# Kernel tuning notes

Measured on AMD Instinct MI355X. Metric: run time of the kernel, lower is better.

Reference implementation:

```python
import jax, jax.numpy as jnp
import numpy as np

# dims: B batch, N tokens (64x64 grid), D slot/feature dim, H heads, HD head_dim
B, N, D = 32, 4096, 256
H, HD = 4, 64            # H * HD == qkv_size == D
S = 16                   # num slots
GH = 128                 # grid-encoder MLP hidden size
MH = 1024                # slot MLP hidden size
NUM_ITER = 3
EPS = 1e-8               # module epsilon
LN_EPS = 1e-6            # flax LayerNorm default


def _ln(x, s, b):
    m = jnp.mean(x, -1, keepdims=True)
    v = jnp.mean(jnp.square(x - m), -1, keepdims=True)
    return (x - m) * jax.lax.rsqrt(v + LN_EPS) * s + b


def setup_inputs() -> dict:
    key = jax.random.key(0)
    ks = jax.random.split(key, 16)
    g = lambda i, shape, scale: jax.random.normal(ks[i], shape, jnp.float32) * scale
    return {
        "slots": g(0, (B, S, D), 1.0),
        "inputs": g(1, (B, N, D + 2), 1.0),  # last 2 channels = coordinate grid
        "ln_in_s": jnp.ones((D,), jnp.float32), "ln_in_b": jnp.zeros((D,), jnp.float32),
        "Wk": g(2, (D, H, HD), D ** -0.5),
        "Wv": g(3, (D, H, HD), D ** -0.5),
        "Wp": g(4, (2, H, HD), 0.5),
        "ge_ln_s": jnp.ones((HD,), jnp.float32), "ge_ln_b": jnp.zeros((HD,), jnp.float32),
        "ge_W1": g(5, (HD, GH), HD ** -0.5), "ge_b1": jnp.zeros((GH,), jnp.float32),
        "ge_W2": g(6, (GH, HD), GH ** -0.5), "ge_b2": jnp.zeros((HD,), jnp.float32),
        "lnq_s": jnp.ones((D,), jnp.float32), "lnq_b": jnp.zeros((D,), jnp.float32),
        "Wq": g(7, (D, H, HD), D ** -0.5),
        "Wo": g(8, (H, HD, D), D ** -0.5),
        "gru_Wi": g(9, (D, 3 * D), D ** -0.5), "gru_bi": jnp.zeros((3 * D,), jnp.float32),
        "gru_Wh": g(10, (D, 3 * D), D ** -0.5), "gru_bhn": jnp.zeros((D,), jnp.float32),
        "mlp_ln_s": jnp.ones((D,), jnp.float32), "mlp_ln_b": jnp.zeros((D,), jnp.float32),
        "mlp_W1": g(11, (D, MH), D ** -0.5), "mlp_b1": jnp.zeros((MH,), jnp.float32),
        "mlp_W2": g(12, (MH, D), MH ** -0.5), "mlp_b2": jnp.zeros((D,), jnp.float32),
    }


def reference(slots, inputs, ln_in_s, ln_in_b, Wk, Wv, Wp, ge_ln_s, ge_ln_b,
              ge_W1, ge_b1, ge_W2, ge_b2, lnq_s, lnq_b, Wq, Wo,
              gru_Wi, gru_bi, gru_Wh, gru_bhn,
              mlp_ln_s, mlp_ln_b, mlp_W1, mlp_b1, mlp_W2, mlp_b2):
    feats, grid = inputs[..., :-2], inputs[..., -2:]
    x = _ln(feats, ln_in_s, ln_in_b)                         # [B,N,D] input pre-norm

    def grid_enc(y):                                          # MLP, pre-LN, no residual
        h = _ln(y, ge_ln_s, ge_ln_b)
        h = jax.nn.relu(h @ ge_W1 + ge_b1)
        return h @ ge_W2 + ge_b2

    p = jnp.einsum('bng,ghe->bnhe', grid, Wp)                 # grid projector
    k = grid_enc(jnp.einsum('bnd,dhe->bnhe', x, Wk) + p)      # [B,N,H,HD]
    v = grid_enc(jnp.einsum('bnd,dhe->bnhe', x, Wv) + p)      # [B,N,H,HD]

    scale = HD ** -0.5
    for _ in range(NUM_ITER):
        sn = _ln(slots, lnq_s, lnq_b)
        q = jnp.einsum('bsd,dhe->bshe', sn, Wq) * scale       # [B,S,H,HD]
        attn = jnp.einsum('bqhe,bkhe->bhqk', q, k)            # [B,H,S,N]
        attn = jax.nn.softmax(attn, axis=-2)                  # inverted: over slots
        attn = attn / (jnp.sum(attn, -1, keepdims=True) + EPS)  # renormalize over keys
        upd = jnp.einsum('bhqk,bkhe->bqhe', attn, v)          # [B,S,H,HD]
        upd = jnp.einsum('bqhe,hed->bqd', upd, Wo)            # multi-head merge -> [B,S,D]
        # flax GRUCell: hidden = slots, input = upd
        gi = upd @ gru_Wi + gru_bi
        gh = slots @ gru_Wh
        ir, iz, inn = jnp.split(gi, 3, -1)
        hr, hz, hn = jnp.split(gh, 3, -1)
        r = jax.nn.sigmoid(ir + hr)
        z = jax.nn.sigmoid(iz + hz)
        n = jnp.tanh(inn + r * (hn + gru_bhn))
        slots = (1.0 - z) * n + z * slots
        # residual pre-LN MLP
        h = _ln(slots, mlp_ln_s, mlp_ln_b)
        h = jax.nn.relu(h @ mlp_W1 + mlp_b1) @ mlp_W2 + mlp_b2
        slots = slots + h
    return slots
```

## Files before the change

### kernel.cpp

```cpp
#include <hip/hip_runtime.h>

using u16 = unsigned short;
using u32 = unsigned int;

#define Bn 32
#define Nn 4096
#define Dn 256
#define Hn 4
#define HDn 64
#define Sn 16

typedef __bf16 bf16x8 __attribute__((ext_vector_type(8)));
typedef float  f32x4  __attribute__((ext_vector_type(4)));

#define MFMA16(a,b,c) __builtin_amdgcn_mfma_f32_16x16x32_bf16((a),(b),(c),0,0,0)

__device__ __forceinline__ float bf2f(u16 u){ u32 x=((u32)u)<<16; float f; __builtin_memcpy(&f,&x,4); return f; }
__device__ __forceinline__ u16 f2bf(float f){ __bf16 h=(__bf16)f; u16 u; __builtin_memcpy(&u,&h,2); return u; }
__device__ __forceinline__ u32 pack2(float a,float b){ return (u32)f2bf(a)|((u32)f2bf(b)<<16); }
__device__ __forceinline__ float sigm(float x){ x=fminf(fmaxf(x,-30.f),30.f); return 1.f/(1.f+__expf(-x)); }
__device__ __forceinline__ float tanhfast(float x){ x=fminf(fmaxf(x,-15.f),15.f); float t=__expf(-2.f*x); return (1.f-t)/(1.f+t); }
__device__ __forceinline__ float gld(const void* p, int idx, bool f32){
  return f32 ? ((const float*)p)[idx] : bf2f(((const u16*)p)[idx]);
}
__device__ __forceinline__ bool is_f32(const u32* flagw){ return *flagw == 0x3F800000u; }

#define PB_LNS 0
#define PB_LNB 256
#define PB_WP 512
#define PB_GES 1024
#define PB_GEB 1088
#define PB_GB1 1152
#define PB_GB2 1280
#define PB_LQS 1344
#define PB_LQB 1600
#define PB_GBI 1856
#define PB_GBHN 2624
#define PB_MLS 2880
#define PB_MLB 3136
#define PB_MB1 3392
#define PB_MB2 4416
#define PB_TOT 4672

__global__ __launch_bounds__(256) void k_prep(
  const void* __restrict__ Wk, const void* __restrict__ Wv,
  const void* __restrict__ gW1, const void* __restrict__ gW2,
  const void* __restrict__ Wq, const void* __restrict__ Wo,
  const void* __restrict__ Wi, const void* __restrict__ Wh,
  const void* __restrict__ mW1, const void* __restrict__ mW2,
  const void* __restrict__ slots_in,
  const void* __restrict__ ln_s, const void* __restrict__ ln_b, const void* __restrict__ Wp,
  const void* __restrict__ ge_s, const void* __restrict__ ge_b,
  const void* __restrict__ geb1, const void* __restrict__ geb2,
  const void* __restrict__ lnqs, const void* __restrict__ lnqb,
  const void* __restrict__ gbi, const void* __restrict__ gbhn,
  const void* __restrict__ mls, const void* __restrict__ mlb,
  const void* __restrict__ mb1, const void* __restrict__ mb2,
  u16* __restrict__ Wcat_t, u16* __restrict__ Wq_t, u16* __restrict__ W1t,
  u16* __restrict__ W2t, u16* __restrict__ Wo_t, u16* __restrict__ Wi_t,
  u16* __restrict__ Wh_t, u16* __restrict__ mW1t, u16* __restrict__ mW2t,
  float* __restrict__ slots_cur, float* __restrict__ pb)
{
  bool f32 = is_f32((const u32*)ln_s);
  int idx = blockIdx.x*256 + threadIdx.x;
  if (idx < 65536){ int o=idx>>8,d=idx&255; Wcat_t[idx]=f2bf(gld(Wk,d*256+o,f32)); return; } idx-=65536;
  if (idx < 65536){ int o=idx>>8,d=idx&255; Wcat_t[65536+idx]=f2bf(gld(Wv,d*256+o,f32)); return; } idx-=65536;
  if (idx < 8192){ int n=idx>>6,k=idx&63; W1t[idx]=f2bf(gld(gW1,k*128+n,f32)); return; } idx-=8192;
  if (idx < 8192){ int n=idx>>7,k=idx&127; W2t[idx]=f2bf(gld(gW2,k*64+n,f32)); return; } idx-=8192;
  if (idx < 65536){ int o=idx>>8,d=idx&255; Wq_t[idx]=f2bf(gld(Wq,d*256+o,f32)); return; } idx-=65536;
  if (idx < 65536){ int d=idx>>8,he=idx&255; Wo_t[idx]=f2bf(gld(Wo,he*256+d,f32)); return; } idx-=65536;
  if (idx < 196608){ int n=idx>>8,k=idx&255; Wi_t[idx]=f2bf(gld(Wi,k*768+n,f32)); return; } idx-=196608;
  if (idx < 196608){ int n=idx>>8,k=idx&255; Wh_t[idx]=f2bf(gld(Wh,k*768+n,f32)); return; } idx-=196608;
  if (idx < 262144){ int n=idx>>8,k=idx&255; mW1t[idx]=f2bf(gld(mW1,k*1024+n,f32)); return; } idx-=262144;
  if (idx < 262144){ int n=idx>>10,k=idx&1023; mW2t[idx]=f2bf(gld(mW2,k*256+n,f32)); return; } idx-=262144;
  if (idx < 131072){ slots_cur[idx]=gld(slots_in,idx,f32); return; } idx-=131072;
  if (idx < 256){ pb[PB_LNS+idx]=gld(ln_s,idx,f32); return; } idx-=256;
  if (idx < 256){ pb[PB_LNB+idx]=gld(ln_b,idx,f32); return; } idx-=256;
  if (idx < 512){ pb[PB_WP+idx]=gld(Wp,idx,f32); return; } idx-=512;
  if (idx < 64){ pb[PB_GES+idx]=gld(ge_s,idx,f32); return; } idx-=64;
  if (idx < 64){ pb[PB_GEB+idx]=gld(ge_b,idx,f32); return; } idx-=64;
  if (idx < 128){ pb[PB_GB1+idx]=gld(geb1,idx,f32); return; } idx-=128;
  if (idx < 64){ pb[PB_GB2+idx]=gld(geb2,idx,f32); return; } idx-=64;
  if (idx < 256){ pb[PB_LQS+idx]=gld(lnqs,idx,f32); return; } idx-=256;
  if (idx < 256){ pb[PB_LQB+idx]=gld(lnqb,idx,f32); return; } idx-=256;
  if (idx < 768){ pb[PB_GBI+idx]=gld(gbi,idx,f32); return; } idx-=768;
  if (idx < 256){ pb[PB_GBHN+idx]=gld(gbhn,idx,f32); return; } idx-=256;
  if (idx < 256){ pb[PB_MLS+idx]=gld(mls,idx,f32); return; } idx-=256;
  if (idx < 256){ pb[PB_MLB+idx]=gld(mlb,idx,f32); return; } idx-=256;
  if (idx < 1024){ pb[PB_MB1+idx]=gld(mb1,idx,f32); return; } idx-=1024;
  if (idx < 256){ pb[PB_MB2+idx]=gld(mb2,idx,f32); return; }
}

__global__ __launch_bounds__(256) void k_feat(
  const void* __restrict__ inputs, const u32* __restrict__ flagw,
  const float* __restrict__ pb,
  const u16* __restrict__ Wcat_t, const u16* __restrict__ W1t_g, const u16* __restrict__ W2t_g,
  u16* __restrict__ Kb, u16* __restrict__ Vb)
{
  __shared__ __align__(16) char sm[56832];
  u16* x_lds = (u16*)sm;
  u16* kp    = (u16*)(sm+16896);
  u16* h_b   = (u16*)(sm+33792);
  u16* stg   = (u16*)(sm+33792);
  float* misc= (float*)(sm+51200);
  float* lnS = misc;      float* lnB = misc+256;
  float* wp0 = misc+512;  float* wp1 = misc+768;
  float* geS = misc+1024; float* geB = misc+1088;
  float* gB1 = misc+1152; float* gB2 = misc+1280;
  float* gxy = misc+1344;

  int tid = threadIdx.x;
  int batch = blockIdx.x >> 7;
  int n0 = (blockIdx.x & 127) << 5;
  bool f32 = is_f32(flagw);

  lnS[tid]=pb[PB_LNS+tid]; lnB[tid]=pb[PB_LNB+tid];
  wp0[tid]=pb[PB_WP+tid];  wp1[tid]=pb[PB_WP+256+tid];
  if (tid < 64){ geS[tid]=pb[PB_GES+tid]; geB[tid]=pb[PB_GEB+tid]; gB2[tid]=pb[PB_GB2+tid]; }
  if (tid < 128) gB1[tid]=pb[PB_GB1+tid];
  __syncthreads();

  {
    int row = tid>>3, seg = tid&7;
    size_t rowbase = ((size_t)(batch*Nn + n0 + row))*258;
    float v[32]; float sum=0.f, ssq=0.f;
    if (f32){
      const float2* ip = (const float2*)((const float*)inputs + rowbase + seg*32);
      #pragma unroll
      for (int i=0;i<16;i++){ float2 t=ip[i]; v[2*i]=t.x; v[2*i+1]=t.y; sum+=t.x+t.y; ssq+=t.x*t.x+t.y*t.y; }
      if (seg==0){
        const float* gp = (const float*)inputs + rowbase + 256;
        gxy[row*2]=gp[0]; gxy[row*2+1]=gp[1];
      }
    } else {
      const u32* ip = (const u32*)inputs + ((rowbase + seg*32)>>1);
      #pragma unroll
      for (int i=0;i<16;i++){ u32 u=ip[i]; float a=bf2f((u16)(u&0xffff)), b=bf2f((u16)(u>>16));
        v[2*i]=a; v[2*i+1]=b; sum+=a+b; ssq+=a*a+b*b; }
      if (seg==0){
        u32 u = *((const u32*)inputs + ((rowbase + 256)>>1));
        gxy[row*2]=bf2f((u16)(u&0xffff)); gxy[row*2+1]=bf2f((u16)(u>>16));
      }
    }
    sum += __shfl_xor(sum,1); sum += __shfl_xor(sum,2); sum += __shfl_xor(sum,4);
    ssq += __shfl_xor(ssq,1); ssq += __shfl_xor(ssq,2); ssq += __shfl_xor(ssq,4);
    float m = sum*(1.f/256.f);
    float var = ssq*(1.f/256.f) - m*m;
    float rs = rsqrtf(var + 1e-6f);
    u32* xw = (u32*)(x_lds + row*264 + seg*32);
    #pragma unroll
    for (int i=0;i<16;i++){
      int c = seg*32 + 2*i;
      float a=(v[2*i]-m)*rs*lnS[c]+lnB[c];
      float b=(v[2*i+1]-m)*rs*lnS[c+1]+lnB[c+1];
      xw[i]=pack2(a,b);
    }
  }
  __syncthreads();

  int wv = tid>>6, lane = tid&63, quad = lane>>4, l15 = lane&15;

  for (int pass=0; pass<2; pass++){
    f32x4 acc[2][4];
    #pragma unroll
    for (int mi=0;mi<2;mi++)
      #pragma unroll
      for (int j=0;j<4;j++) acc[mi][j]=(f32x4){0,0,0,0};
    const u16* Bbase = Wcat_t + pass*65536;
    #pragma unroll
    for (int ks=0; ks<8; ks++){
      bf16x8 a[2], bb[4];
      #pragma unroll
      for (int mi=0;mi<2;mi++) a[mi] = *(const bf16x8*)(x_lds + (mi*16+l15)*264 + ks*32 + quad*8);
      #pragma unroll
      for (int j=0;j<4;j++) bb[j] = *(const bf16x8*)(Bbase + ((wv*4+j)*16+l15)*256 + ks*32 + quad*8);
      #pragma unroll
      for (int mi=0;mi<2;mi++)
        #pragma unroll
        for (int j=0;j<4;j++) acc[mi][j] = MFMA16(a[mi], bb[j], acc[mi][j]);
    }
    #pragma unroll
    for (int j=0;j<4;j++){
      int col = wv*64 + j*16 + l15;
      float w0 = wp0[col], w1 = wp1[col];
      #pragma unroll
      for (int mi=0;mi<2;mi++)
        #pragma unroll
        for (int r=0;r<4;r++){
          int rw = mi*16 + quad*4 + r;
          float val = acc[mi][j][r] + gxy[rw*2]*w0 + gxy[rw*2+1]*w1;
          kp[rw*264 + col] = f2bf(val);
        }
    }
    __syncthreads();

    {
      int g = tid>>1, halfe = tid&1;
      int token = g>>2, hd = g&3;
      u32* ptr = (u32*)(kp + token*264 + hd*64 + halfe*32);
      float vv[32]; float sum=0.f, ssq=0.f;
      #pragma unroll
      for (int i=0;i<16;i++){ u32 u=ptr[i]; float a=bf2f((u16)(u&0xffff)), b=bf2f((u16)(u>>16));
        vv[2*i]=a; vv[2*i+1]=b; sum+=a+b; ssq+=a*a+b*b; }
      sum += __shfl_xor(sum,1); ssq += __shfl_xor(ssq,1);
      float m = sum*(1.f/64.f);
      float var = ssq*(1.f/64.f) - m*m;
      float rs = rsqrtf(var + 1e-6f);
      #pragma unroll
      for (int i=0;i<16;i++){
        int e = halfe*32 + 2*i;
        float a=(vv[2*i]-m)*rs*geS[e]+geB[e];
        float b=(vv[2*i+1]-m)*rs*geS[e+1]+geB[e+1];
        ptr[i]=pack2(a,b);
      }
    }
    __syncthreads();

    int mtb = (wv>>1)*2;
    for (int half=0; half<2; half++){
      int hbase = half*64;
      int ntb = (wv&1)*4;
      f32x4 e1[2][4];
      #pragma unroll
      for (int mi=0;mi<2;mi++)
        #pragma unroll
        for (int nj=0;nj<4;nj++) e1[mi][nj]=(f32x4){0,0,0,0};
      #pragma unroll
      for (int ks=0; ks<2; ks++){
        bf16x8 a[2], bb[4];
        #pragma unroll
        for (int mi=0;mi<2;mi++){
          int g = hbase + (mtb+mi)*16 + l15;
          a[mi] = *(const bf16x8*)(kp + (g>>2)*264 + (g&3)*64 + ks*32 + quad*8);
        }
        #pragma unroll
        for (int nj=0;nj<4;nj++) bb[nj] = *(const bf16x8*)(W1t_g + ((ntb+nj)*16+l15)*64 + ks*32 + quad*8);
        #pragma unroll
        for (int mi=0;mi<2;mi++)
          #pragma unroll
          for (int nj=0;nj<4;nj++) e1[mi][nj] = MFMA16(a[mi], bb[nj], e1[mi][nj]);
      }
      #pragma unroll
      for (int nj=0;nj<4;nj++){
        int col = (ntb+nj)*16 + l15;
        float b1 = gB1[col];
        #pragma unroll
        for (int mi=0;mi<2;mi++)
          #pragma unroll
          for (int r=0;r<4;r++){
            int rw = (mtb+mi)*16 + quad*4 + r;
            h_b[rw*136 + col] = f2bf(fmaxf(e1[mi][nj][r]+b1, 0.f));
          }
      }
      __syncthreads();
      int ntb2 = (wv&1)*2;
      f32x4 e2[2][2];
      #pragma unroll
      for (int mi=0;mi<2;mi++)
        #pragma unroll
        for (int nj=0;nj<2;nj++) e2[mi][nj]=(f32x4){0,0,0,0};
      #pragma unroll
      for (int ks=0; ks<4; ks++){
        bf16x8 a[2], bb[2];
        #pragma unroll
        for (int mi=0;mi<2;mi++) a[mi] = *(const bf16x8*)(h_b + ((mtb+mi)*16+l15)*136 + ks*32 + quad*8);
        #pragma unroll
        for (int nj=0;nj<2;nj++) bb[nj] = *(const bf16x8*)(W2t_g + ((ntb2+nj)*16+l15)*128 + ks*32 + quad*8);
        #pragma unroll
        for (int mi=0;mi<2;mi++)
          #pragma unroll
          for (int nj=0;nj<2;nj++) e2[mi][nj] = MFMA16(a[mi], bb[nj], e2[mi][nj]);
      }
      __syncthreads();
      #pragma unroll
      for (int nj=0;nj<2;nj++){
        int e = (ntb2+nj)*16 + l15;
        float b2 = gB2[e];
        #pragma unroll
        for (int mi=0;mi<2;mi++)
          #pragma unroll
          for (int r=0;r<4;r++){
            int g = hbase + (mtb+mi)*16 + quad*4 + r;
            int hd = g&3, rowl = (g>>2)&15;
            float val = e2[mi][nj][r] + b2;
            if (pass==0) stg[hd*16*72 + rowl*72 + e] = f2bf(val);
            else         stg[hd*64*24 + e*24 + rowl] = f2bf(val);
          }
      }
      __syncthreads();
      if (pass==0){
        int hd = tid>>6, rowl = (tid>>2)&15, sg = tid&3;
        const uint4* s = (const uint4*)(stg + hd*1152 + rowl*72 + sg*16);
        uint4 q0 = s[0], q1 = s[1];
        u16* dst = Kb + ((size_t)((batch*Hn+hd)*Nn + n0 + half*16 + rowl))*64 + sg*16;
        ((uint4*)dst)[0]=q0; ((uint4*)dst)[1]=q1;
      } else {
        int hd = tid>>6, e = tid&63;
        const uint4* s = (const uint4*)(stg + hd*1536 + e*24);
        uint4 q0 = s[0], q1 = s[1];
        u16* dst = Vb + ((size_t)((batch*Hn+hd)*HDn + e))*Nn + n0 + half*16;
        ((uint4*)dst)[0]=q0; ((uint4*)dst)[1]=q1;
      }
      __syncthreads();
    }
  }
}

__global__ __launch_bounds__(256) void k_attn(
  const float* __restrict__ slots_cur, const float* __restrict__ pb,
  const u16* __restrict__ Wq_t, const u16* __restrict__ Kb, const u16* __restrict__ Vb,
  float* __restrict__ num_part, float* __restrict__ den_part)
{
  __shared__ u16 sn[16*264];
  __shared__ u16 qld[16*72];
  __shared__ u16 pld[4][16*40];
  int tid = threadIdx.x;
  int chunk = blockIdx.x, h = blockIdx.y, b = blockIdx.z;

  {
    int rowq = tid>>4, li = tid&15;
    const float* sp = slots_cur + ((size_t)(b*16+rowq))*256 + li*16;
    float v[16]; float sum=0.f, ssq=0.f;
    #pragma unroll
    for (int i=0;i<16;i++){ float x=sp[i]; v[i]=x; sum+=x; ssq+=x*x; }
    sum += __shfl_xor(sum,1); sum += __shfl_xor(sum,2); sum += __shfl_xor(sum,4); sum += __shfl_xor(sum,8);
    ssq += __shfl_xor(ssq,1); ssq += __shfl_xor(ssq,2); ssq += __shfl_xor(ssq,4); ssq += __shfl_xor(ssq,8);
    float m = sum*(1.f/256.f);
    float var = ssq*(1.f/256.f) - m*m;
    float rs = rsqrtf(var + 1e-6f);
    u32* dst = (u32*)(sn + rowq*264 + li*16);
    #pragma unroll
    for (int i=0;i<8;i++){
      int c = li*16 + 2*i;
      float a=(v[2*i]-m)*rs*pb[PB_LQS+c]+pb[PB_LQB+c];
      float bval=(v[2*i+1]-m)*rs*pb[PB_LQS+c+1]+pb[PB_LQB+c+1];
      dst[i]=pack2(a,bval);
    }
  }
  __syncthreads();

  int wv = tid>>6, lane = tid&63, quad = lane>>4, l15 = lane&15;
  {
    f32x4 qa = (f32x4){0,0,0,0};
    #pragma unroll
    for (int ks=0; ks<8; ks++){
      bf16x8 a = *(const bf16x8*)(sn + l15*264 + ks*32 + quad*8);
      bf16x8 bb = *(const bf16x8*)(Wq_t + (h*64 + wv*16 + l15)*256 + ks*32 + quad*8);
      qa = MFMA16(a, bb, qa);
    }
    #pragma unroll
    for (int r=0;r<4;r++) qld[(quad*4+r)*72 + wv*16 + l15] = f2bf(qa[r]*0.125f);
  }
  __syncthreads();

  bf16x8 qb0 = *(const bf16x8*)(qld + l15*72 + quad*8);
  bf16x8 qb1 = *(const bf16x8*)(qld + l15*72 + 32 + quad*8);
  f32x4 vacc[4];
  #pragma unroll
  for (int nt=0;nt<4;nt++) vacc[nt]=(f32x4){0,0,0,0};
  float denp = 0.f;
  const u16* Kbase = Kb + ((size_t)(b*Hn+h))*Nn*64;
  const u16* Vbase = Vb + ((size_t)(b*Hn+h))*64*Nn;
  u16* myp = pld[wv];

  for (int it=0; it<8; it++){
    int g0 = chunk*1024 + wv*256 + it*32;
    float pn[2][4];
    #pragma unroll
    for (int s=0;s<2;s++){
      bf16x8 a0 = *(const bf16x8*)(Kbase + (size_t)(g0+s*16+l15)*64 + quad*8);
      bf16x8 a1 = *(const bf16x8*)(Kbase + (size_t)(g0+s*16+l15)*64 + 32 + quad*8);
      f32x4 c = (f32x4){0,0,0,0};
      c = MFMA16(a0, qb0, c);
      c = MFMA16(a1, qb1, c);
      #pragma unroll
      for (int r=0;r<4;r++){
        float sc = c[r];
        float mx = sc;
        mx = fmaxf(mx, __shfl_xor(mx,1)); mx = fmaxf(mx, __shfl_xor(mx,2));
        mx = fmaxf(mx, __shfl_xor(mx,4)); mx = fmaxf(mx, __shfl_xor(mx,8));
        float e = __expf(sc - mx);
        float t = e;
        t += __shfl_xor(t,1); t += __shfl_xor(t,2); t += __shfl_xor(t,4); t += __shfl_xor(t,8);
        float p = e / t;
        float pr = bf2f(f2bf(p));
        pn[s][r] = p; denp += pr;
      }
    }
    __syncthreads();
    #pragma unroll
    for (int s=0;s<2;s++){
      uint2 w; w.x = pack2(pn[s][0], pn[s][1]); w.y = pack2(pn[s][2], pn[s][3]);
      *(uint2*)(myp + l15*40 + s*16 + quad*4) = w;
    }
    __syncthreads();
    bf16x8 pa = *(const bf16x8*)(myp + l15*40 + quad*8);
    #pragma unroll
    for (int nt=0;nt<4;nt++){
      bf16x8 vb = *(const bf16x8*)(Vbase + (size_t)(nt*16+l15)*Nn + g0 + quad*8);
      vacc[nt] = MFMA16(pa, vb, vacc[nt]);
    }
  }
  denp += __shfl_xor(denp,16); denp += __shfl_xor(denp,32);
  int wc = chunk*4 + wv;
  float* np = num_part + ((size_t)((b*Hn+h)*16 + wc))*1024;
  #pragma unroll
  for (int nt=0;nt<4;nt++)
    #pragma unroll
    for (int r=0;r<4;r++) np[(quad*4+r)*64 + nt*16 + l15] = vacc[nt][r];
  if (lane < 16) den_part[((b*Hn+h)*16 + wc)*16 + lane] = denp;
}

__global__ __launch_bounds__(256) void k_slot(
  float* __restrict__ slots_cur, const float* __restrict__ num_part, const float* __restrict__ den_part,
  const u16* __restrict__ Wo_t, const u16* __restrict__ Wi_t, const u16* __restrict__ Wh_t,
  const u16* __restrict__ mW1t, const u16* __restrict__ mW2t,
  const float* __restrict__ pb, const u32* __restrict__ flagw,
  void* __restrict__ out)
{
  __shared__ __align__(16) char sm[59392];
  u16* upd_b    = (u16*)(sm);
  u16* updo_b   = (u16*)(sm+8448);
  float* slots_f= (float*)(sm+16896);
  u16* hr_b     = (u16*)(sm);
  u16* slhm_b   = (u16*)(sm+33792);
  float* snew_f = (float*)(sm+42240);
  float* den_l  = (float*)(sm+59136);
  int tid = threadIdx.x, b = blockIdx.x;
  bool of32 = is_f32(flagw);

  {
    const float* sp = slots_cur + (size_t)b*4096;
    for (int i=tid; i<4096; i+=256){
      int sl=i>>8, c=i&255; float v=sp[i];
      slots_f[sl*264+c]=v; slhm_b[sl*264+c]=f2bf(v);
    }
  }
  if (tid < 64){
    int h=tid>>4, sl=tid&15; float s=0.f;
    for (int wc=0; wc<16; wc++) s += den_part[((b*Hn+h)*16+wc)*16 + sl];
    den_l[tid] = s + 1e-8f;
  }
  __syncthreads();
  {
    int he = tid, h = he>>6, e = he&63;
    for (int sl=0; sl<16; sl++){
      float s=0.f;
      for (int wc=0; wc<16; wc++)
        s += num_part[((size_t)((b*Hn+h)*16+wc))*1024 + sl*64 + e];
      upd_b[sl*264 + he] = f2bf(s / den_l[h*16+sl]);
    }
  }
  __syncthreads();

  int wv = tid>>6, lane = tid&63, quad = lane>>4, l15 = lane&15;
  {
    f32x4 acc[4];
    #pragma unroll
    for (int j=0;j<4;j++) acc[j]=(f32x4){0,0,0,0};
    #pragma unroll
    for (int ks=0; ks<8; ks++){
      bf16x8 a = *(const bf16x8*)(upd_b + l15*264 + ks*32 + quad*8);
      #pragma unroll
      for (int j=0;j<4;j++){
        bf16x8 bb = *(const bf16x8*)(Wo_t + ((wv*4+j)*16+l15)*256 + ks*32 + quad*8);
        acc[j] = MFMA16(a, bb, acc[j]);
      }
    }
    #pragma unroll
    for (int j=0;j<4;j++)
      #pragma unroll
      for (int r=0;r<4;r++) updo_b[(quad*4+r)*264 + (wv*4+j)*16 + l15] = f2bf(acc[j][r]);
  }
  __syncthreads();
  {
    f32x4 gi[3][4], gh[3][4];
    #pragma unroll
    for (int g=0;g<3;g++)
      #pragma unroll
      for (int j=0;j<4;j++){ gi[g][j]=(f32x4){0,0,0,0}; gh[g][j]=(f32x4){0,0,0,0}; }
    #pragma unroll
    for (int ks=0; ks<8; ks++){
      bf16x8 au = *(const bf16x8*)(updo_b + l15*264 + ks*32 + quad*8);
      bf16x8 as = *(const bf16x8*)(slhm_b + l15*264 + ks*32 + quad*8);
      #pragma unroll
      for (int g=0;g<3;g++)
        #pragma unroll
        for (int j=0;j<4;j++){
          int colg = g*256 + (wv*4+j)*16 + l15;
          bf16x8 bi_ = *(const bf16x8*)(Wi_t + (size_t)colg*256 + ks*32 + quad*8);
          bf16x8 bh_ = *(const bf16x8*)(Wh_t + (size_t)colg*256 + ks*32 + quad*8);
          gi[g][j] = MFMA16(au, bi_, gi[g][j]);
          gh[g][j] = MFMA16(as, bh_, gh[g][j]);
        }
    }
    #pragma unroll
    for (int j=0;j<4;j++){
      int dcol = (wv*4+j)*16 + l15;
      float bir = pb[PB_GBI+dcol], biz = pb[PB_GBI+256+dcol], bin = pb[PB_GBI+512+dcol];
      float bhn = pb[PB_GBHN+dcol];
      #pragma unroll
      for (int r=0;r<4;r++){
        int sl = quad*4 + r;
        float ir = gi[0][j][r]+bir, iz = gi[1][j][r]+biz, inn = gi[2][j][r]+bin;
        float hrr = gh[0][j][r], hz = gh[1][j][r], hn = gh[2][j][r];
        float rg = sigm(ir + hrr);
        float z  = sigm(iz + hz);
        float nn = tanhfast(inn + rg*(hn + bhn));
        float old = slots_f[sl*264 + dcol];
        snew_f[sl*264 + dcol] = (1.f - z)*nn + z*old;
      }
    }
  }
  __syncthreads();
  {
    int sl = tid>>4, li = tid&15;
    float v[16]; float sum=0.f, ssq=0.f;
    #pragma unroll
    for (int i=0;i<16;i++){ float x=snew_f[sl*264 + li*16 + i]; v[i]=x; sum+=x; ssq+=x*x; }
    sum += __shfl_xor(sum,1); sum += __shfl_xor(sum,2); sum += __shfl_xor(sum,4); sum += __shfl_xor(sum,8);
    ssq += __shfl_xor(ssq,1); ssq += __shfl_xor(ssq,2); ssq += __shfl_xor(ssq,4); ssq += __shfl_xor(ssq,8);
    float m = sum*(1.f/256.f);
    float var = ssq*(1.f/256.f) - m*m;
    float rs = rsqrtf(var + 1e-6f);
    #pragma unroll
    for (int i=0;i<16;i++){
      int c = li*16 + i;
      slhm_b[sl*264+c] = f2bf((v[i]-m)*rs*pb[PB_MLS+c] + pb[PB_MLB+c]);
    }
  }
  __syncthreads();
  {
    f32x4 acc[16];
    #pragma unroll
    for (int j=0;j<16;j++) acc[j]=(f32x4){0,0,0,0};
    #pragma unroll
    for (int ks=0; ks<8; ks++){
      bf16x8 a = *(const bf16x8*)(slhm_b + l15*264 + ks*32 + quad*8);
      #pragma unroll
      for (int j=0;j<16;j++){
        int col = (wv*16+j)*16 + l15;
        bf16x8 bb = *(const bf16x8*)(mW1t + (size_t)col*256 + ks*32 + quad*8);
        acc[j] = MFMA16(a, bb, acc[j]);
      }
    }
    __syncthreads();
    #pragma unroll
    for (int j=0;j<16;j++){
      int col = (wv*16+j)*16 + l15;
      float b1 = pb[PB_MB1+col];
      #pragma unroll
      for (int r=0;r<4;r++) hr_b[(quad*4+r)*1032 + col] = f2bf(fmaxf(acc[j][r]+b1, 0.f));
    }
  }
  __syncthreads();
  {
    f32x4 acc[4];
    #pragma unroll
    for (int j=0;j<4;j++) acc[j]=(f32x4){0,0,0,0};
    #pragma unroll
    for (int ks=0; ks<32; ks++){
      bf16x8 a = *(const bf16x8*)(hr_b + l15*1032 + ks*32 + quad*8);
      #pragma unroll
      for (int j=0;j<4;j++){
        int col = (wv*4+j)*16 + l15;
        bf16x8 bb = *(const bf16x8*)(mW2t + (size_t)col*1024 + ks*32 + quad*8);
        acc[j] = MFMA16(a, bb, acc[j]);
      }
    }
    #pragma unroll
    for (int j=0;j<4;j++)
      #pragma unroll
      for (int r=0;r<4;r++){
        int col = (wv*4+j)*16 + l15;
        int sl = quad*4 + r;
        float res = snew_f[sl*264+col] + acc[j][r] + pb[PB_MB2+col];
        size_t oi = (size_t)b*4096 + sl*256 + col;
        slots_cur[oi] = res;
        if (of32) ((float*)out)[oi] = res;
        else      ((u16*)out)[oi] = f2bf(res);
      }
  }
}

extern "C" void kernel_launch(void* const* d_in, const int* in_sizes, int n_in,
                              void* d_out, int out_size, void* d_ws, size_t ws_size,
                              hipStream_t stream)
{
  const void* slots_in = d_in[0];
  const void* inputs   = d_in[1];
  const void* ln_in_s  = d_in[2];
  const void* ln_in_b  = d_in[3];
  const void* Wk       = d_in[4];
  const void* Wv       = d_in[5];
  const void* Wp       = d_in[6];
  const void* ge_ln_s  = d_in[7];
  const void* ge_ln_b  = d_in[8];
  const void* ge_W1    = d_in[9];
  const void* ge_b1    = d_in[10];
  const void* ge_W2    = d_in[11];
  const void* ge_b2    = d_in[12];
  const void* lnq_s    = d_in[13];
  const void* lnq_b    = d_in[14];
  const void* Wq       = d_in[15];
  const void* Wo       = d_in[16];
  const void* gru_Wi   = d_in[17];
  const void* gru_bi   = d_in[18];
  const void* gru_Wh   = d_in[19];
  const void* gru_bhn  = d_in[20];
  const void* mlp_ln_s = d_in[21];
  const void* mlp_ln_b = d_in[22];
  const void* mlp_W1   = d_in[23];
  const void* mlp_b1   = d_in[24];
  const void* mlp_W2   = d_in[25];
  const void* mlp_b2   = d_in[26];

  char* ws = (char*)d_ws;
  u16* Wcat_t = (u16*)(ws + 0);
  u16* Wq_t   = (u16*)(ws + 262144);
  u16* W1t    = (u16*)(ws + 393216);
  u16* W2t    = (u16*)(ws + 409600);
  u16* Wo_t   = (u16*)(ws + 425984);
  u16* Wi_t   = (u16*)(ws + 557056);
  u16* Wh_t   = (u16*)(ws + 950272);
  u16* mW1t   = (u16*)(ws + 1343488);
  u16* mW2t   = (u16*)(ws + 1867776);
  u16* Kb     = (u16*)(ws + 2392064);
  u16* Vb     = (u16*)(ws + 69500928);
  float* slots_cur = (float*)(ws + 136609792);
  float* num_part  = (float*)(ws + 137134080);
  float* den_part  = (float*)(ws + 145522688);
  float* pb        = (float*)(ws + 145653760);

  const u32* flagw = (const u32*)ln_in_s;

  k_prep<<<5203, 256, 0, stream>>>(Wk, Wv, ge_W1, ge_W2, Wq, Wo, gru_Wi, gru_Wh,
                                   mlp_W1, mlp_W2, slots_in,
                                   ln_in_s, ln_in_b, Wp, ge_ln_s, ge_ln_b, ge_b1, ge_b2,
                                   lnq_s, lnq_b, gru_bi, gru_bhn, mlp_ln_s, mlp_ln_b,
                                   mlp_b1, mlp_b2,
                                   Wcat_t, Wq_t, W1t, W2t, Wo_t, Wi_t, Wh_t, mW1t, mW2t,
                                   slots_cur, pb);

  k_feat<<<4096, 256, 0, stream>>>(inputs, flagw, pb, Wcat_t, W1t, W2t, Kb, Vb);

  for (int iter=0; iter<3; iter++){
    k_attn<<<dim3(4,4,32), 256, 0, stream>>>(slots_cur, pb, Wq_t, Kb, Vb,
                                             num_part, den_part);
    k_slot<<<32, 256, 0, stream>>>(slots_cur, num_part, den_part, Wo_t, Wi_t, Wh_t,
                                   mW1t, mW2t, pb, flagw, d_out);
  }
}
```

Before: 928.4 us.

## Restructure feature kernel so each wave owns one head, removing block barriers

Measured after the change: 943.0 us. No clear change (+1.6%).

```diff
diff --git a/kernel.cpp b/kernel.cpp
--- a/kernel.cpp
+++ b/kernel.cpp
@@ -14,6 +14,7 @@
 typedef float  f32x4  __attribute__((ext_vector_type(4)));
 
 #define MFMA16(a,b,c) __builtin_amdgcn_mfma_f32_16x16x32_bf16((a),(b),(c),0,0,0)
+#define CFENCE() __asm__ __volatile__("" ::: "memory")
 
 __device__ __forceinline__ float bf2f(u16 u){ u32 x=((u32)u)<<16; float f; __builtin_memcpy(&f,&x,4); return f; }
 __device__ __forceinline__ u16 f2bf(float f){ __bf16 h=(__bf16)f; u16 u; __builtin_memcpy(&u,&h,2); return u; }
@@ -91,18 +92,15 @@
   if (idx < 256){ pb[PB_MB2+idx]=gld(mb2,idx,f32); return; }
 }
 
-__global__ __launch_bounds__(256) void k_feat(
+__global__ __launch_bounds__(256, 3) void k_feat(
   const void* __restrict__ inputs, const u32* __restrict__ flagw,
   const float* __restrict__ pb,
   const u16* __restrict__ Wcat_t, const u16* __restrict__ W1t_g, const u16* __restrict__ W2t_g,
   u16* __restrict__ Kb, u16* __restrict__ Vb)
 {
-  __shared__ __align__(16) char sm[56832];
+  __shared__ __align__(16) char sm[53248];
   u16* x_lds = (u16*)sm;
-  u16* kp    = (u16*)(sm+16896);
-  u16* h_b   = (u16*)(sm+33792);
-  u16* stg   = (u16*)(sm+33792);
-  float* misc= (float*)(sm+51200);
+  float* misc = (float*)(sm + 16896);
   float* lnS = misc;      float* lnB = misc+256;
   float* wp0 = misc+512;  float* wp1 = misc+768;
   float* geS = misc+1024; float* geB = misc+1088;
@@ -159,150 +157,149 @@
   __syncthreads();
 
   int wv = tid>>6, lane = tid&63, quad = lane>>4, l15 = lane&15;
+  int h = wv;
+  u16* bufA = (u16*)(sm + 22528 + wv*7680);
+  u16* bufB = (u16*)(sm + 22528 + wv*7680 + 5120);
+
+  float g0[2], g1[2];
+  g0[0]=gxy[l15*2];      g1[0]=gxy[l15*2+1];
+  g0[1]=gxy[(16+l15)*2]; g1[1]=gxy[(16+l15)*2+1];
 
   for (int pass=0; pass<2; pass++){
-    f32x4 acc[2][4];
-    #pragma unroll
-    for (int mi=0;mi<2;mi++)
-      #pragma unroll
-      for (int j=0;j<4;j++) acc[mi][j]=(f32x4){0,0,0,0};
-    const u16* Bbase = Wcat_t + pass*65536;
+    f32x4 acc[4][2];
+    #pragma unroll
+    for (int mi=0;mi<4;mi++){ acc[mi][0]=(f32x4){0,0,0,0}; acc[mi][1]=(f32x4){0,0,0,0}; }
+    const u16* Wb = Wcat_t + pass*65536;
     #pragma unroll
     for (int ks=0; ks<8; ks++){
-      bf16x8 a[2], bb[4];
-      #pragma unroll
-      for (int mi=0;mi<2;mi++) a[mi] = *(const bf16x8*)(x_lds + (mi*16+l15)*264 + ks*32 + quad*8);
-      #pragma unroll
-      for (int j=0;j<4;j++) bb[j] = *(const bf16x8*)(Bbase + ((wv*4+j)*16+l15)*256 + ks*32 + quad*8);
-      #pragma unroll
-      for (int mi=0;mi<2;mi++)
+      bf16x8 bx[2];
+      #pragma unroll
+      for (int nt=0;nt<2;nt++) bx[nt] = *(const bf16x8*)(x_lds + (nt*16+l15)*264 + ks*32 + quad*8);
+      #pragma unroll
+      for (int mi=0;mi<4;mi++){
+        bf16x8 aw = *(const bf16x8*)(Wb + (h*64+mi*16+l15)*256 + ks*32 + quad*8);
+        acc[mi][0] = MFMA16(aw, bx[0], acc[mi][0]);
+        acc[mi][1] = MFMA16(aw, bx[1], acc[mi][1]);
+      }
+    }
+    float vv[4][2][4];
+    float s0=0.f, s1=0.f, q0s=0.f, q1s=0.f;
+    #pragma unroll
+    for (int mi=0;mi<4;mi++)
+      #pragma unroll
+      for (int r=0;r<4;r++){
+        int eg = h*64 + mi*16 + quad*4 + r;
+        float w0 = wp0[eg], w1 = wp1[eg];
+        float a = acc[mi][0][r] + g0[0]*w0 + g1[0]*w1;
+        float b = acc[mi][1][r] + g0[1]*w0 + g1[1]*w1;
+        vv[mi][0][r]=a; vv[mi][1][r]=b;
+        s0+=a; q0s+=a*a; s1+=b; q1s+=b*b;
+      }
+    s0 += __shfl_xor(s0,16); s0 += __shfl_xor(s0,32);
+    s1 += __shfl_xor(s1,16); s1 += __shfl_xor(s1,32);
+    q0s += __shfl_xor(q0s,16); q0s += __shfl_xor(q0s,32);
+    q1s += __shfl_xor(q1s,16); q1s += __shfl_xor(q1s,32);
+    float m0 = s0*(1.f/64.f), m1 = s1*(1.f/64.f);
+    float rs0 = rsqrtf(q0s*(1.f/64.f) - m0*m0 + 1e-6f);
+    float rs1 = rsqrtf(q1s*(1.f/64.f) - m1*m1 + 1e-6f);
+    CFENCE();
+    #pragma unroll
+    for (int mi=0;mi<4;mi++)
+      #pragma unroll
+      for (int rp=0;rp<2;rp++){
+        int el0 = mi*16 + quad*4 + 2*rp;
+        float ga = geS[el0], gb_ = geB[el0], gc = geS[el0+1], gd = geB[el0+1];
+        u32 wA = pack2((vv[mi][0][2*rp]-m0)*rs0*ga+gb_, (vv[mi][0][2*rp+1]-m0)*rs0*gc+gd);
+        u32 wB = pack2((vv[mi][1][2*rp]-m1)*rs1*ga+gb_, (vv[mi][1][2*rp+1]-m1)*rs1*gc+gd);
+        *(u32*)(bufA + (l15)*72 + el0)      = wA;
+        *(u32*)(bufA + (16+l15)*72 + el0)   = wB;
+      }
+    CFENCE();
+    f32x4 acc2[4][2];
+    #pragma unroll
+    for (int mi=0;mi<4;mi++){ acc2[mi][0]=(f32x4){0,0,0,0}; acc2[mi][1]=(f32x4){0,0,0,0}; }
+    for (int qq=0; qq<4; qq++){
+      f32x4 a1[2][2];
+      #pragma unroll
+      for (int ml=0;ml<2;ml++){ a1[ml][0]=(f32x4){0,0,0,0}; a1[ml][1]=(f32x4){0,0,0,0}; }
+      #pragma unroll
+      for (int ks2=0; ks2<2; ks2++){
+        bf16x8 bh[2];
         #pragma unroll
-        for (int j=0;j<4;j++) acc[mi][j] = MFMA16(a[mi], bb[j], acc[mi][j]);
-    }
-    #pragma unroll
-    for (int j=0;j<4;j++){
-      int col = wv*64 + j*16 + l15;
-      float w0 = wp0[col], w1 = wp1[col];
-      #pragma unroll
-      for (int mi=0;mi<2;mi++)
+        for (int nt=0;nt<2;nt++) bh[nt] = *(const bf16x8*)(bufA + (nt*16+l15)*72 + ks2*32 + quad*8);
+        #pragma unroll
+        for (int ml=0;ml<2;ml++){
+          bf16x8 aW = *(const bf16x8*)(W1t_g + ((qq*2+ml)*16+l15)*64 + ks2*32 + quad*8);
+          a1[ml][0] = MFMA16(aW, bh[0], a1[ml][0]);
+          a1[ml][1] = MFMA16(aW, bh[1], a1[ml][1]);
+        }
+      }
+      CFENCE();
+      #pragma unroll
+      for (int ml=0;ml<2;ml++)
+        #pragma unroll
+        for (int rp=0;rp<2;rp++){
+          int ghl = ml*16 + quad*4 + 2*rp;
+          float b1a = gB1[qq*32+ghl], b1b = gB1[qq*32+ghl+1];
+          u32 wA = pack2(fmaxf(a1[ml][0][2*rp]+b1a,0.f), fmaxf(a1[ml][0][2*rp+1]+b1b,0.f));
+          u32 wB = pack2(fmaxf(a1[ml][1][2*rp]+b1a,0.f), fmaxf(a1[ml][1][2*rp+1]+b1b,0.f));
+          *(u32*)(bufB + (l15)*40 + ghl)    = wA;
+          *(u32*)(bufB + (16+l15)*40 + ghl) = wB;
+        }
+      CFENCE();
+      bf16x8 bq[2];
+      #pragma unroll
+      for (int nt=0;nt<2;nt++) bq[nt] = *(const bf16x8*)(bufB + (nt*16+l15)*40 + quad*8);
+      #pragma unroll
+      for (int mi=0;mi<4;mi++){
+        bf16x8 a2 = *(const bf16x8*)(W2t_g + (mi*16+l15)*128 + qq*32 + quad*8);
+        acc2[mi][0] = MFMA16(a2, bq[0], acc2[mi][0]);
+        acc2[mi][1] = MFMA16(a2, bq[1], acc2[mi][1]);
+      }
+    }
+    CFENCE();
+    if (pass==0){
+      #pragma unroll
+      for (int mi=0;mi<4;mi++)
+        #pragma unroll
+        for (int rp=0;rp<2;rp++){
+          int el0 = mi*16 + quad*4 + 2*rp;
+          float b2a = gB2[el0], b2b = gB2[el0+1];
+          u32 wA = pack2(acc2[mi][0][2*rp]+b2a, acc2[mi][0][2*rp+1]+b2b);
+          u32 wB = pack2(acc2[mi][1][2*rp]+b2a, acc2[mi][1][2*rp+1]+b2b);
+          *(u32*)(bufA + (l15)*72 + el0)    = wA;
+          *(u32*)(bufA + (16+l15)*72 + el0) = wB;
+        }
+      CFENCE();
+      int row = lane>>1, half = lane&1;
+      uint4 t0 = *(const uint4*)(bufA + row*72 + half*32);
+      uint4 t1 = *(const uint4*)(bufA + row*72 + half*32 + 8);
+      uint4 t2 = *(const uint4*)(bufA + row*72 + half*32 + 16);
+      uint4 t3 = *(const uint4*)(bufA + row*72 + half*32 + 24);
+      u16* dst = Kb + ((size_t)((batch*Hn+h)*Nn + n0 + row))*64 + half*32;
+      ((uint4*)dst)[0]=t0; ((uint4*)dst)[1]=t1;
+      u16* dst2 = dst + 16;
+      ((uint4*)(dst2))[0]=t2; ((uint4*)(dst2))[1]=t3;
+    } else {
+      #pragma unroll
+      for (int mi=0;mi<4;mi++)
         #pragma unroll
         for (int r=0;r<4;r++){
-          int rw = mi*16 + quad*4 + r;
-          float val = acc[mi][j][r] + gxy[rw*2]*w0 + gxy[rw*2+1]*w1;
-          kp[rw*264 + col] = f2bf(val);
+          int e2 = mi*16 + quad*4 + r;
+          float b2 = gB2[e2];
+          bufA[e2*40 + l15]      = f2bf(acc2[mi][0][r]+b2);
+          bufA[e2*40 + 16 + l15] = f2bf(acc2[mi][1][r]+b2);
         }
-    }
-    __syncthreads();
-
-    {
-      int g = tid>>1, halfe = tid&1;
-      int token = g>>2, hd = g&3;
-      u32* ptr = (u32*)(kp + token*264 + hd*64 + halfe*32);
-      float vv[32]; float sum=0.f, ssq=0.f;
-      #pragma unroll
-      for (int i=0;i<16;i++){ u32 u=ptr[i]; float a=bf2f((u16)(u&0xffff)), b=bf2f((u16)(u>>16));
-        vv[2*i]=a; vv[2*i+1]=b; sum+=a+b; ssq+=a*a+b*b; }
-      sum += __shfl_xor(sum,1); ssq += __shfl_xor(ssq,1);
-      float m = sum*(1.f/64.f);
-      float var = ssq*(1.f/64.f) - m*m;
-      float rs = rsqrtf(var + 1e-6f);
-      #pragma unroll
-      for (int i=0;i<16;i++){
-        int e = halfe*32 + 2*i;
-        float a=(vv[2*i]-m)*rs*geS[e]+geB[e];
-        float b=(vv[2*i+1]-m)*rs*geS[e+1]+geB[e+1];
-        ptr[i]=pack2(a,b);
-      }
-    }
-    __syncthreads();
-
-    int mtb = (wv>>1)*2;
-    for (int half=0; half<2; half++){
-      int hbase = half*64;
-      int ntb = (wv&1)*4;
-      f32x4 e1[2][4];
-      #pragma unroll
-      for (int mi=0;mi<2;mi++)
-        #pragma unroll
-        for (int nj=0;nj<4;nj++) e1[mi][nj]=(f32x4){0,0,0,0};
-      #pragma unroll
-      for (int ks=0; ks<2; ks++){
-        bf16x8 a[2], bb[4];
-        #pragma unroll
-        for (int mi=0;mi<2;mi++){
-          int g = hbase + (mtb+mi)*16 + l15;
-          a[mi] = *(const bf16x8*)(kp + (g>>2)*264 + (g&3)*64 + ks*32 + quad*8);
-        }
-        #pragma unroll
-        for (int nj=0;nj<4;nj++) bb[nj] = *(const bf16x8*)(W1t_g + ((ntb+nj)*16+l15)*64 + ks*32 + quad*8);
-        #pragma unroll
-        for (int mi=0;mi<2;mi++)
-          #pragma unroll
-          for (int nj=0;nj<4;nj++) e1[mi][nj] = MFMA16(a[mi], bb[nj], e1[mi][nj]);
-      }
-      #pragma unroll
-      for (int nj=0;nj<4;nj++){
-        int col = (ntb+nj)*16 + l15;
-        float b1 = gB1[col];
-        #pragma unroll
-        for (int mi=0;mi<2;mi++)
-          #pragma unroll
-          for (int r=0;r<4;r++){
-            int rw = (mtb+mi)*16 + quad*4 + r;
-            h_b[rw*136 + col] = f2bf(fmaxf(e1[mi][nj][r]+b1, 0.f));
-          }
-      }
-      __syncthreads();
-      int ntb2 = (wv&1)*2;
-      f32x4 e2[2][2];
-      #pragma unroll
-      for (int mi=0;mi<2;mi++)
-        #pragma unroll
-        for (int nj=0;nj<2;nj++) e2[mi][nj]=(f32x4){0,0,0,0};
-      #pragma unroll
-      for (int ks=0; ks<4; ks++){
-        bf16x8 a[2], bb[2];
-        #pragma unroll
-        for (int mi=0;mi<2;mi++) a[mi] = *(const bf16x8*)(h_b + ((mtb+mi)*16+l15)*136 + ks*32 + quad*8);
-        #pragma unroll
-        for (int nj=0;nj<2;nj++) bb[nj] = *(const bf16x8*)(W2t_g + ((ntb2+nj)*16+l15)*128 + ks*32 + quad*8);
-        #pragma unroll
-        for (int mi=0;mi<2;mi++)
-          #pragma unroll
-          for (int nj=0;nj<2;nj++) e2[mi][nj] = MFMA16(a[mi], bb[nj], e2[mi][nj]);
-      }
-      __syncthreads();
-      #pragma unroll
-      for (int nj=0;nj<2;nj++){
-        int e = (ntb2+nj)*16 + l15;
-        float b2 = gB2[e];
-        #pragma unroll
-        for (int mi=0;mi<2;mi++)
-          #pragma unroll
-          for (int r=0;r<4;r++){
-            int g = hbase + (mtb+mi)*16 + quad*4 + r;
-            int hd = g&3, rowl = (g>>2)&15;
-            float val = e2[mi][nj][r] + b2;
-            if (pass==0) stg[hd*16*72 + rowl*72 + e] = f2bf(val);
-            else         stg[hd*64*24 + e*24 + rowl] = f2bf(val);
-          }
-      }
-      __syncthreads();
-      if (pass==0){
-        int hd = tid>>6, rowl = (tid>>2)&15, sg = tid&3;
-        const uint4* s = (const uint4*)(stg + hd*1152 + rowl*72 + sg*16);
-        uint4 q0 = s[0], q1 = s[1];
-        u16* dst = Kb + ((size_t)((batch*Hn+hd)*Nn + n0 + half*16 + rowl))*64 + sg*16;
-        ((uint4*)dst)[0]=q0; ((uint4*)dst)[1]=q1;
-      } else {
-        int hd = tid>>6, e = tid&63;
-        const uint4* s = (const uint4*)(stg + hd*1536 + e*24);
-        uint4 q0 = s[0], q1 = s[1];
-        u16* dst = Vb + ((size_t)((batch*Hn+hd)*HDn + e))*Nn + n0 + half*16;
-        ((uint4*)dst)[0]=q0; ((uint4*)dst)[1]=q1;
-      }
-      __syncthreads();
-    }
+      CFENCE();
+      int e = lane;
+      uint4 t0 = *(const uint4*)(bufA + e*40);
+      uint4 t1 = *(const uint4*)(bufA + e*40 + 8);
+      uint4 t2 = *(const uint4*)(bufA + e*40 + 16);
+      uint4 t3 = *(const uint4*)(bufA + e*40 + 24);
+      u16* dst = Vb + ((size_t)((batch*Hn+h)*HDn + e))*Nn + n0;
+      ((uint4*)dst)[0]=t0; ((uint4*)dst)[1]=t1; ((uint4*)dst)[2]=t2; ((uint4*)dst)[3]=t3;
+    }
+    CFENCE();
   }
 }
 
@@ -387,13 +384,13 @@
         pn[s][r] = p; denp += pr;
       }
     }
-    __syncthreads();
+    CFENCE();
     #pragma unroll
     for (int s=0;s<2;s++){
       uint2 w; w.x = pack2(pn[s][0], pn[s][1]); w.y = pack2(pn[s][2], pn[s][3]);
       *(uint2*)(myp + l15*40 + s*16 + quad*4) = w;
     }
-    __syncthreads();
+    CFENCE();
     bf16x8 pa = *(const bf16x8*)(myp + l15*40 + quad*8);
     #pragma unroll
     for (int nt=0;nt<4;nt++){
```
